# Kernel optimization log

Measured on AMD Instinct MI355X. Metric: run time of the kernel, lower is better.

Reference implementation:

```python
import jax, jax.numpy as jnp
import numpy as np

B, T, NF, C, H, TOPK = 4, 8, 8192, 384, 12, 32
D = C // H
SCALE = D ** -0.5  # qk_scale=None -> head_dim**-0.5


def setup_inputs() -> dict:
    key = jax.random.key(0)
    ks = jax.random.split(key, 4)
    x = jax.random.normal(ks[0], (B, T + NF, C), jnp.float32)
    qs_w = jax.random.normal(ks[1], (T, C, C), jnp.float32) * (C ** -0.5)
    kv_w = jax.random.normal(ks[2], (C, 2 * C), jnp.float32) * (C ** -0.5)
    experts_w = jax.random.normal(ks[3], (T, C, C), jnp.float32) * (C ** -0.5)
    return {"x": x, "qs_w": qs_w, "kv_w": kv_w, "experts_w": experts_w}


def reference(x, qs_w, kv_w, experts_w):
    # x: [B, T+NF, C]; first T tokens are task tokens, rest are feature tokens
    feature = x[:, T:, :]                                          # [B,NF,C]
    kv = (feature @ kv_w).reshape(B, NF, 2, H, D)                  # out dim splits [2,H,D]
    k = kv[:, :, 0].transpose(0, 2, 1, 3)                          # [B,H,NF,D]
    v = kv[:, :, 1].transpose(0, 2, 1, 3)                          # [B,H,NF,D]
    # per-task query linears (no bias), one task token each
    q = jnp.einsum('btc,tco->bto', x[:, :T, :], qs_w)              # [B,T,C]
    q = q.reshape(B, T, H, D).transpose(0, 2, 1, 3)                # [B,H,T,D]
    attn = jnp.einsum('bhtd,bhnd->bhtn', q, k) * SCALE             # [B,H,T,NF]
    vals, idx = jax.lax.top_k(attn, TOPK)                          # [B,H,T,K]
    w = jax.nn.softmax(vals, axis=-1)                              # softmax over top-k only
    # attn_token = (scatter(topk softmax) @ v) == weighted gather of v rows
    v_g = jnp.take_along_axis(v[:, :, None], idx[..., None], axis=3)   # [B,H,T,K,D]
    attn_token = jnp.einsum('bhtk,bhtkd->bhtd', w, v_g)
    attn_token = attn_token.transpose(0, 2, 1, 3).reshape(B, T, C)     # [B,T,C]
    # gather raw feature tokens at top-k indices, weight, scatter into padded zeros
    fm = feature.reshape(B, NF, H, D).transpose(0, 2, 1, 3)        # [B,H,NF,D]
    f_g = jnp.take_along_axis(fm[:, :, None], idx[..., None], axis=3) * w[..., None]  # [B,H,T,K,D]
    bi = jnp.arange(B)[:, None, None, None]
    hi = jnp.arange(H)[None, :, None, None]
    ti = jnp.arange(T)[None, None, :, None]
    # topk indices are unique per row -> set is well-defined
    feature_pad = jnp.zeros((B, H, T, NF, D), x.dtype).at[bi, hi, ti, idx].set(f_g)
    feature_pad = feature_pad.transpose(0, 2, 3, 1, 4).reshape(B, T, NF, C)  # [B,T,NF,C]
    # per-task expert linears; einsum with ones weight == sum over tasks
    feature_out = jnp.einsum('btnc,tco->bno', feature_pad, experts_w)  # [B,NF,C]
    token_out = jnp.einsum('btc,tco->bto', attn_token, experts_w)      # [B,T,C]
    return jnp.concatenate([token_out, feature_out], axis=1)          # [B,T+NF,C]
```

## Files before the change

### kernel.cpp

```cpp
#include <hip/hip_runtime.h>
#include <hip/hip_bf16.h>
#include <math.h>

#define B 4
#define T 8
#define NF 8192
#define C 384
#define H 12
#define TOPK 32
#define D 32
#define STOT (T + NF)
#define R (H * T)
#define KSEL 48
#define SCALE 0.17677669529663687f

typedef unsigned int uint;
typedef unsigned short ushort;
typedef short bf16x8 __attribute__((ext_vector_type(8)));
typedef float f32x4 __attribute__((ext_vector_type(4)));

__device__ __forceinline__ ushort bf16u(float a) {
  return __builtin_bit_cast(ushort, __float2bfloat16(a));
}

__device__ __forceinline__ ushort f32_key(float s) {
  uint kb = bf16u(s);
  kb ^= (kb & 0x8000u) ? 0xFFFFu : 0x8000u;
  return (ushort)kb;
}

__global__ __launch_bounds__(256) void ta_qproj_kernel(
    const float* __restrict__ x, const float* __restrict__ qs_w,
    float* __restrict__ q_part) {
  int t = blockIdx.x;
  int o0 = blockIdx.y * 64;
  int z = blockIdx.z;
  int tid = threadIdx.x;
  int o = tid & 63, ks = tid >> 6;
  __shared__ float xs[B][192];
  __shared__ float part[4][B][64];
  if (tid < 192) {
    int b = tid / 48, j4 = (tid % 48) * 4;
    *reinterpret_cast<float4*>(&xs[b][j4]) =
        *reinterpret_cast<const float4*>(x + ((size_t)b * STOT + t) * C + z * 192 + j4);
  }
  __syncthreads();
  float a0 = 0.f, a1 = 0.f, a2 = 0.f, a3 = 0.f;
  const float* w = qs_w + (size_t)t * C * C + (size_t)(z * 192 + ks * 48) * C + o0 + o;
#pragma unroll 8
  for (int c = 0; c < 48; ++c) {
    float wv = w[(size_t)c * C];
    int cj = ks * 48 + c;
    a0 += xs[0][cj] * wv;
    a1 += xs[1][cj] * wv;
    a2 += xs[2][cj] * wv;
    a3 += xs[3][cj] * wv;
  }
  part[ks][0][o] = a0; part[ks][1][o] = a1;
  part[ks][2][o] = a2; part[ks][3][o] = a3;
  __syncthreads();
  {
    int b = tid >> 6, oo = tid & 63;
    float s = part[0][b][oo] + part[1][b][oo] + part[2][b][oo] + part[3][b][oo];
    q_part[(((size_t)z * B + b) * T + t) * C + o0 + oo] = s;
  }
}

__global__ __launch_bounds__(384) void ta_fold_kernel(
    const float* __restrict__ q_part, const float* __restrict__ kv_w,
    float* __restrict__ qk_f32, ushort* __restrict__ qk_bf) {
  int b = blockIdx.x / H, h = blockIdx.x % H;
  int tid = threadIdx.x;
  __shared__ float kS[C][33];
  __shared__ float qh[T][D];
  if (tid < T * D) {
    int t = tid >> 5, d = tid & 31;
    qh[t][d] = q_part[((size_t)b * T + t) * C + h * D + d] +
               q_part[(((size_t)B + b) * T + t) * C + h * D + d];
  }
  for (int j = tid; j < C * 8; j += 384) {
    int c = j >> 3, d4 = (j & 7) * 4;
    float4 v = *reinterpret_cast<const float4*>(
        kv_w + (size_t)c * (2 * C) + h * D + d4);
    kS[c][d4 + 0] = v.x; kS[c][d4 + 1] = v.y;
    kS[c][d4 + 2] = v.z; kS[c][d4 + 3] = v.w;
  }
  __syncthreads();
  float acc[T] = {0.f, 0.f, 0.f, 0.f, 0.f, 0.f, 0.f, 0.f};
#pragma unroll
  for (int d = 0; d < D; ++d) {
    float kv = kS[tid][d];
#pragma unroll
    for (int t = 0; t < T; ++t) acc[t] += qh[t][d] * kv;
  }
#pragma unroll
  for (int t = 0; t < T; ++t) {
    size_t off = ((size_t)b * R + (size_t)h * T + t) * C + tid;
    float a = acc[t];
    qk_f32[off] = a;
    qk_bf[off] = bf16u(a);
  }
}

__global__ __launch_bounds__(256) void ta_scores_kernel(
    const float* __restrict__ x, const ushort* __restrict__ qk_bf,
    ushort* __restrict__ keys) {
  int b = blockIdx.y;
  int n0 = blockIdx.x * 64;
  int tid = threadIdx.x;
  int lane = tid & 63, w = tid >> 6;
  int row16 = lane & 15, kg = lane >> 4;
  __shared__ ushort fS[64][72];
  __shared__ ushort qS[96][72];
  f32x4 acc[6];
#pragma unroll
  for (int i = 0; i < 6; ++i) acc[i] = (f32x4){0.f, 0.f, 0.f, 0.f};

  const float* xb = x + ((size_t)b * STOT + T + n0) * C;
  const ushort* qb = qk_bf + (size_t)b * R * C;

  int frow = tid >> 2, fcg = (tid & 3) * 8;

#pragma unroll 1
  for (int c0 = 0; c0 < C; c0 += 32) {
    {
      const float* src = xb + (size_t)frow * C + c0 + fcg;
      float4 v0 = *reinterpret_cast<const float4*>(src);
      float4 v1 = *reinterpret_cast<const float4*>(src + 4);
      uint4 p;
      p.x = (uint)bf16u(v0.x) | ((uint)bf16u(v0.y) << 16);
      p.y = (uint)bf16u(v0.z) | ((uint)bf16u(v0.w) << 16);
      p.z = (uint)bf16u(v1.x) | ((uint)bf16u(v1.y) << 16);
      p.w = (uint)bf16u(v1.z) | ((uint)bf16u(v1.w) << 16);
      *reinterpret_cast<uint4*>(&fS[frow][fcg]) = p;
    }
#pragma unroll
    for (int s = 0; s < 2; ++s) {
      int u = tid + 256 * s;
      if (u < 384) {
        int row = u >> 2, cg = (u & 3) * 8;
        uint4 v = *reinterpret_cast<const uint4*>(qb + (size_t)row * C + c0 + cg);
        *reinterpret_cast<uint4*>(&qS[row][cg]) = v;
      }
    }
    __syncthreads();
    bf16x8 bfr = *reinterpret_cast<const bf16x8*>(&fS[w * 16 + row16][kg * 8]);
#pragma unroll
    for (int i = 0; i < 6; ++i) {
      bf16x8 afr = *reinterpret_cast<const bf16x8*>(&qS[i * 16 + row16][kg * 8]);
      acc[i] = __builtin_amdgcn_mfma_f32_16x16x32_bf16(afr, bfr, acc[i], 0, 0, 0);
    }
    __syncthreads();
  }
  int n = n0 + w * 16 + row16;
#pragma unroll
  for (int i = 0; i < 6; ++i) {
    int rbase = i * 16 + kg * 4;
#pragma unroll
    for (int reg = 0; reg < 4; ++reg) {
      keys[((size_t)b * R + rbase + reg) * NF + n] = f32_key(acc[i][reg] * SCALE);
    }
  }
}

__global__ __launch_bounds__(384) void ta_selres_kernel(
    const ushort* __restrict__ keys, const float* __restrict__ x,
    const float* __restrict__ qk_f32, float* __restrict__ w_buf,
    int* __restrict__ idx_buf, float4* __restrict__ out4) {
  int rr = blockIdx.x;
  int b = rr / R;
  int tid = threadIdx.x;
  int lane = tid & 63, wvi = tid >> 6;
  __shared__ __align__(16) ushort su[NF];
  __shared__ uint histW[6][256];
  __shared__ uint sh_prefix, sh_above, cgt, ceq;
  __shared__ int gt_list[KSEL];
  __shared__ int eq_list[128];
  __shared__ int il[KSEL];
  __shared__ float sv[KSEL];
  __shared__ int rkS[KSEL];
  __shared__ float qS[C];
  __shared__ float smax, esum;

  {
    const uint4* src = reinterpret_cast<const uint4*>(keys + (size_t)rr * NF);
    uint4* dst = reinterpret_cast<uint4*>(su);
    for (int j = tid; j < NF / 8; j += 384) dst[j] = src[j];
  }
  {
    float4 z = {0.f, 0.f, 0.f, 0.f};
    float4* dst = out4 + (size_t)rr * (B * STOT * C / 4 / (B * R));
    for (int j = tid; j < B * STOT * C / 4 / (B * R); j += 384) dst[j] = z;
  }
  qS[tid] = qk_f32[(size_t)rr * C + tid];
  for (int i = tid; i < 6 * 256; i += 384) (&histW[0][0])[i] = 0;
  if (tid == 0) { cgt = 0; ceq = 0; }
  __syncthreads();

  for (int i = tid; i < NF; i += 384) atomicAdd(&histW[wvi][su[i] >> 8], 1u);
  __syncthreads();
  if (tid < 64) {
    uint h0 = 0, h1 = 0, h2 = 0, h3 = 0;
#pragma unroll
    for (int wq = 0; wq < 6; ++wq) {
      h0 += histW[wq][4 * lane + 0];
      h1 += histW[wq][4 * lane + 1];
      h2 += histW[wq][4 * lane + 2];
      h3 += histW[wq][4 * lane + 3];
    }
    uint lsum = h0 + h1 + h2 + h3;
    uint suf = lsum;
#pragma unroll
    for (int off = 1; off < 64; off <<= 1) {
      uint o = __shfl_down(suf, off);
      if (lane + off < 64) suf += o;
    }
    uint gn3 = suf - lsum;
    uint ge3 = gn3 + h3;
    uint ge2 = ge3 + h2;
    uint ge1 = ge2 + h1;
    uint ge0 = ge1 + h0;
    const uint need = KSEL;
    if (ge0 >= need && ge1 < need) { sh_prefix = 4 * lane + 0; sh_above = ge1; }
    if (ge1 >= need && ge2 < need) { sh_prefix = 4 * lane + 1; sh_above = ge2; }
    if (ge2 >= need && ge3 < need) { sh_prefix = 4 * lane + 2; sh_above = ge3; }
    if (ge3 >= need && gn3 < need) { sh_prefix = 4 * lane + 3; sh_above = gn3; }
  }
  __syncthreads();
  uint pref1 = sh_prefix, ab1 = sh_above;
  for (int i = tid; i < 6 * 256; i += 384) (&histW[0][0])[i] = 0;
  __syncthreads();
  for (int i = tid; i < NF; i += 384) {
    uint u = su[i];
    if ((u >> 8) == pref1) atomicAdd(&histW[wvi][u & 255], 1u);
  }
  __syncthreads();
  if (tid < 64) {
    uint h0 = 0, h1 = 0, h2 = 0, h3 = 0;
#pragma unroll
    for (int wq = 0; wq < 6; ++wq) {
      h0 += histW[wq][4 * lane + 0];
      h1 += histW[wq][4 * lane + 1];
      h2 += histW[wq][4 * lane + 2];
      h3 += histW[wq][4 * lane + 3];
    }
    uint lsum = h0 + h1 + h2 + h3;
    uint suf = lsum;
#pragma unroll
    for (int off = 1; off < 64; off <<= 1) {
      uint o = __shfl_down(suf, off);
      if (lane + off < 64) suf += o;
    }
    uint gn3 = suf - lsum;
    uint ge3 = gn3 + h3;
    uint ge2 = ge3 + h2;
    uint ge1 = ge2 + h1;
    uint ge0 = ge1 + h0;
    const uint need = (uint)KSEL - ab1;
    if (ge0 >= need && ge1 < need) { sh_prefix = (pref1 << 8) | (4 * lane + 0); sh_above = ab1 + ge1; }
    if (ge1 >= need && ge2 < need) { sh_prefix = (pref1 << 8) | (4 * lane + 1); sh_above = ab1 + ge2; }
    if (ge2 >= need && ge3 < need) { sh_prefix = (pref1 << 8) | (4 * lane + 2); sh_above = ab1 + ge3; }
    if (ge3 >= need && gn3 < need) { sh_prefix = (pref1 << 8) | (4 * lane + 3); sh_above = ab1 + gn3; }
  }
  __syncthreads();
  uint piv = sh_prefix, ab = sh_above;
  for (int i = tid; i < NF; i += 384) {
    uint u = su[i];
    if (u > piv) {
      uint s = atomicAdd(&cgt, 1u);
      gt_list[s] = i;
    } else if (u == piv) {
      uint s = atomicAdd(&ceq, 1u);
      if (s < 128) eq_list[s] = i;
    }
  }
  __syncthreads();
  if (tid < (int)ab) il[tid] = gt_list[tid];
  {
    uint ne = ceq < 128u ? ceq : 128u;
    if (tid < (int)ne) {
      int my = eq_list[tid];
      int r2 = 0;
      for (uint e = 0; e < ne; ++e) r2 += (eq_list[e] < my);
      if (r2 < (int)((uint)KSEL - ab)) il[ab + r2] = my;
    }
  }
  __syncthreads();

  int k = tid >> 3, j = tid & 7;
  const float* fp = x + ((size_t)b * STOT + T + il[k]) * C + j;
  float s = 0.f;
#pragma unroll 8
  for (int m = 0; m < 48; ++m) s += fp[m * 8] * qS[j + m * 8];
  s += __shfl_down(s, 4);
  s += __shfl_down(s, 2);
  s += __shfl_down(s, 1);
  if (j == 0) sv[k] = s * SCALE;
  __syncthreads();
  if (tid < KSEL) {
    float mys = sv[tid];
    int myn = il[tid];
    int r = 0;
#pragma unroll
    for (int e = 0; e < KSEL; ++e) {
      float se = sv[e];
      r += (se > mys) || (se == mys && il[e] < myn);
    }
    rkS[tid] = r;
    if (r == 0) smax = mys;
  }
  __syncthreads();
  float e = 0.f;
  if (tid < KSEL && rkS[tid] < TOPK) e = expf(sv[tid] - smax);
  if (tid < 64) {
    float t2 = e;
#pragma unroll
    for (int off = 32; off; off >>= 1) t2 += __shfl_down(t2, off);
    if (tid == 0) esum = t2;
  }
  __syncthreads();
  if (tid < KSEL && rkS[tid] < TOPK) {
    w_buf[(size_t)rr * TOPK + rkS[tid]] = e / esum;
    idx_buf[(size_t)rr * TOPK + rkS[tid]] = il[tid];
  }
}

__global__ __launch_bounds__(256) void ta_gvscatter_kernel(
    const float* __restrict__ x, const float* __restrict__ kv_w,
    const float* __restrict__ ew, const float* __restrict__ w_buf,
    const int* __restrict__ idx_buf, float* __restrict__ out) {
  int br = blockIdx.x;
  int t = br % T, h = (br / T) % H, b = br / R;
  int tid = threadIdx.x;
  int k = tid >> 3, dg = tid & 7;
  __shared__ float Fc[TOPK][100];
  __shared__ float Vc[96][36];
  __shared__ float vS[TOPK][36];
  __shared__ float gS[TOPK][36];
  __shared__ __align__(16) float attS[D];
  __shared__ float wl[TOPK];
  __shared__ int il[TOPK];

  if (tid < TOPK) {
    wl[tid] = w_buf[(size_t)br * TOPK + tid];
    il[tid] = idx_buf[(size_t)br * TOPK + tid];
  }
  __syncthreads();
  float4 acc = {0.f, 0.f, 0.f, 0.f};
  int hc = (h * D) / 96;
#pragma unroll 1
  for (int ch = 0; ch < 4; ++ch) {
    int c0 = ch * 96;
    if (ch) __syncthreads();
#pragma unroll
    for (int s = 0; s < 3; ++s) {
      int u = tid + 256 * s;
      int kr = u / 24, c4 = (u % 24) * 4;
      *reinterpret_cast<float4*>(&Fc[kr][c4]) =
          *reinterpret_cast<const float4*>(
              x + ((size_t)b * STOT + T + il[kr]) * C + c0 + c4);
    }
#pragma unroll
    for (int s = 0; s < 3; ++s) {
      int u = tid + 256 * s;
      int cr = u >> 3, d4 = (u & 7) * 4;
      *reinterpret_cast<float4*>(&Vc[cr][d4]) =
          *reinterpret_cast<const float4*>(
              kv_w + (size_t)(c0 + cr) * (2 * C) + C + h * D + d4);
    }
    __syncthreads();
    if (ch == hc) {
      int off = h * D - c0;
      float4 f = *reinterpret_cast<const float4*>(&Fc[k][off + 4 * dg]);
      float wk = wl[k];
      float4 g = {wk * f.x, wk * f.y, wk * f.z, wk * f.w};
      *reinterpret_cast<float4*>(&gS[k][4 * dg]) = g;
    }
#pragma unroll 4
    for (int c = 0; c < 96; c += 4) {
      float4 f4 = *reinterpret_cast<const float4*>(&Fc[k][c]);
      float4 v0 = *reinterpret_cast<const float4*>(&Vc[c + 0][4 * dg]);
      float4 v1 = *reinterpret_cast<const float4*>(&Vc[c + 1][4 * dg]);
      float4 v2 = *reinterpret_cast<const float4*>(&Vc[c + 2][4 * dg]);
      float4 v3 = *reinterpret_cast<const float4*>(&Vc[c + 3][4 * dg]);
      acc.x += f4.x * v0.x + f4.y * v1.x + f4.z * v2.x + f4.w * v3.x;
      acc.y += f4.x * v0.y + f4.y * v1.y + f4.z * v2.y + f4.w * v3.y;
      acc.z += f4.x * v0.z + f4.y * v1.z + f4.z * v2.z + f4.w * v3.z;
      acc.w += f4.x * v0.w + f4.y * v1.w + f4.z * v2.w + f4.w * v3.w;
    }
  }
  *reinterpret_cast<float4*>(&vS[k][4 * dg]) = acc;
  __syncthreads();
  if (tid < D) {
    float a = 0.f;
#pragma unroll
    for (int kk = 0; kk < TOPK; ++kk) a += wl[kk] * vS[kk][tid];
    attS[tid] = a;
  }
  __syncthreads();

  float ewc0[D], ewc1[D];
  const float* ewt = ew + (size_t)t * C * C + (size_t)h * D * C;
#pragma unroll
  for (int dd = 0; dd < D; ++dd) {
    ewc0[dd] = ewt[(size_t)dd * C + tid];
    ewc1[dd] = (tid < 128) ? ewt[(size_t)dd * C + tid + 256] : 0.f;
  }
  size_t obase = (size_t)b * STOT * C;
#pragma unroll 1
  for (int kk = 0; kk < TOPK; ++kk) {
    float y0 = 0.f, y1 = 0.f;
#pragma unroll
    for (int d4 = 0; d4 < D; d4 += 4) {
      float4 g4 = *reinterpret_cast<const float4*>(&gS[kk][d4]);
      y0 += g4.x * ewc0[d4] + g4.y * ewc0[d4 + 1] +
            g4.z * ewc0[d4 + 2] + g4.w * ewc0[d4 + 3];
      y1 += g4.x * ewc1[d4] + g4.y * ewc1[d4 + 1] +
            g4.z * ewc1[d4 + 2] + g4.w * ewc1[d4 + 3];
    }
    size_t row = obase + (size_t)(T + il[kk]) * C;
    atomicAdd(&out[row + tid], y0);
    if (tid < 128) atomicAdd(&out[row + tid + 256], y1);
  }
  {
    float y0 = 0.f, y1 = 0.f;
#pragma unroll
    for (int d4 = 0; d4 < D; d4 += 4) {
      float4 a4 = *reinterpret_cast<const float4*>(attS + d4);
      y0 += a4.x * ewc0[d4] + a4.y * ewc0[d4 + 1] +
            a4.z * ewc0[d4 + 2] + a4.w * ewc0[d4 + 3];
      y1 += a4.x * ewc1[d4] + a4.y * ewc1[d4 + 1] +
            a4.z * ewc1[d4 + 2] + a4.w * ewc1[d4 + 3];
    }
    size_t row = obase + (size_t)t * C;
    atomicAdd(&out[row + tid], y0);
    if (tid < 128) atomicAdd(&out[row + tid + 256], y1);
  }
}

extern "C" void kernel_launch(void* const* d_in, const int* in_sizes, int n_in,
                              void* d_out, int out_size, void* d_ws, size_t ws_size,
                              hipStream_t stream) {
  const float* x = (const float*)d_in[0];
  const float* qs_w = (const float*)d_in[1];
  const float* kv_w = (const float*)d_in[2];
  const float* ew = (const float*)d_in[3];
  float* out = (float*)d_out;

  char* p = (char*)d_ws;
  float* qk_f32 = (float*)p;  p += (size_t)B * R * C * 4;
  ushort* qk_bf = (ushort*)p; p += (size_t)B * R * C * 2;
  ushort* keys = (ushort*)p;  p += (size_t)B * R * NF * 2;
  float* w_buf = (float*)p;   p += (size_t)B * R * TOPK * 4;
  int* idx_buf = (int*)p;     p += (size_t)B * R * TOPK * 4;
  float* q_part = (float*)p;

  dim3 gq(T, C / 64, 2);
  ta_qproj_kernel<<<gq, 256, 0, stream>>>(x, qs_w, q_part);
  ta_fold_kernel<<<B * H, 384, 0, stream>>>(q_part, kv_w, qk_f32, qk_bf);
  dim3 g2(NF / 64, B);
  ta_scores_kernel<<<g2, 256, 0, stream>>>(x, qk_bf, keys);
  ta_selres_kernel<<<B * R, 384, 0, stream>>>(keys, x, qk_f32, w_buf, idx_buf,
                                              (float4*)out);
  ta_gvscatter_kernel<<<B * R, 256, 0, stream>>>(x, kv_w, ew, w_buf, idx_buf, out);
}
```

Before: 88.77 us.

## Fuse top-k selection with gather/scatter kernel and move output zeroing into scores

Merges the selection/softmax kernel and the gather-V/expert-scatter kernel into one 256-thread kernel, with a shared-memory union so the selection buffers and the gather tiles reuse the same LDS. Weights and indices stay in shared memory instead of going through global w_buf/idx_buf, which removes one launch and a round trip through memory. The zeroing of the output moves into the scores kernel's 512 blocks, spreading it across more blocks. In exchange the selection phase runs with fewer threads per block (256 instead of 384), and the fused block's larger LDS use may lower occupancy.

```diff
diff --git a/kernel.cpp b/kernel.cpp
--- a/kernel.cpp
+++ b/kernel.cpp
@@ -104,7 +104,7 @@
 
 __global__ __launch_bounds__(256) void ta_scores_kernel(
     const float* __restrict__ x, const ushort* __restrict__ qk_bf,
-    ushort* __restrict__ keys) {
+    ushort* __restrict__ keys, float4* __restrict__ out4) {
   int b = blockIdx.y;
   int n0 = blockIdx.x * 64;
   int tid = threadIdx.x;
@@ -115,6 +115,14 @@
   f32x4 acc[6];
 #pragma unroll
   for (int i = 0; i < 6; ++i) acc[i] = (f32x4){0.f, 0.f, 0.f, 0.f};
+
+  {
+    const int SL = (B * STOT * C / 4) / 512;
+    int zbid = blockIdx.y * gridDim.x + blockIdx.x;
+    float4 z = {0.f, 0.f, 0.f, 0.f};
+    float4* dst = out4 + (size_t)zbid * SL;
+    for (int j = tid; j < SL; j += 256) dst[j] = z;
+  }
 
   const float* xb = x + ((size_t)b * STOT + T + n0) * C;
   const ushort* qb = qk_bf + (size_t)b * R * C;
@@ -163,50 +171,60 @@
   }
 }
 
-__global__ __launch_bounds__(384) void ta_selres_kernel(
+__global__ __launch_bounds__(256) void ta_selgv_kernel(
     const ushort* __restrict__ keys, const float* __restrict__ x,
-    const float* __restrict__ qk_f32, float* __restrict__ w_buf,
-    int* __restrict__ idx_buf, float4* __restrict__ out4) {
-  int rr = blockIdx.x;
-  int b = rr / R;
+    const float* __restrict__ qk_f32, const float* __restrict__ kv_w,
+    const float* __restrict__ ew, float* __restrict__ out) {
+  int br = blockIdx.x;
+  int t = br % T, h = (br / T) % H, b = br / R;
   int tid = threadIdx.x;
   int lane = tid & 63, wvi = tid >> 6;
-  __shared__ __align__(16) ushort su[NF];
-  __shared__ uint histW[6][256];
+
+  union SM {
+    struct {
+      ushort su[NF];
+      uint histW[4][256];
+      float qS[C];
+      int gt_list[KSEL];
+      int eq_list[128];
+      int il[KSEL];
+      float sv[KSEL];
+      int rkS[KSEL];
+    } a;
+    struct {
+      float Fc[TOPK][100];
+      float Vc[96][36];
+    } g;
+  };
+  __shared__ SM sm;
+  __shared__ float vS[TOPK][36];
+  __shared__ float gS[TOPK][36];
+  __shared__ __align__(16) float attS[D];
+  __shared__ float wl[TOPK];
+  __shared__ int top_il[TOPK];
   __shared__ uint sh_prefix, sh_above, cgt, ceq;
-  __shared__ int gt_list[KSEL];
-  __shared__ int eq_list[128];
-  __shared__ int il[KSEL];
-  __shared__ float sv[KSEL];
-  __shared__ int rkS[KSEL];
-  __shared__ float qS[C];
   __shared__ float smax, esum;
 
   {
-    const uint4* src = reinterpret_cast<const uint4*>(keys + (size_t)rr * NF);
-    uint4* dst = reinterpret_cast<uint4*>(su);
-    for (int j = tid; j < NF / 8; j += 384) dst[j] = src[j];
-  }
-  {
-    float4 z = {0.f, 0.f, 0.f, 0.f};
-    float4* dst = out4 + (size_t)rr * (B * STOT * C / 4 / (B * R));
-    for (int j = tid; j < B * STOT * C / 4 / (B * R); j += 384) dst[j] = z;
-  }
-  qS[tid] = qk_f32[(size_t)rr * C + tid];
-  for (int i = tid; i < 6 * 256; i += 384) (&histW[0][0])[i] = 0;
+    const uint4* src = reinterpret_cast<const uint4*>(keys + (size_t)br * NF);
+    uint4* dst = reinterpret_cast<uint4*>(sm.a.su);
+    for (int j = tid; j < NF / 8; j += 256) dst[j] = src[j];
+  }
+  for (int j = tid; j < C; j += 256) sm.a.qS[j] = qk_f32[(size_t)br * C + j];
+  for (int i = tid; i < 4 * 256; i += 256) (&sm.a.histW[0][0])[i] = 0;
   if (tid == 0) { cgt = 0; ceq = 0; }
   __syncthreads();
 
-  for (int i = tid; i < NF; i += 384) atomicAdd(&histW[wvi][su[i] >> 8], 1u);
+  for (int i = tid; i < NF; i += 256) atomicAdd(&sm.a.histW[wvi][sm.a.su[i] >> 8], 1u);
   __syncthreads();
   if (tid < 64) {
     uint h0 = 0, h1 = 0, h2 = 0, h3 = 0;
 #pragma unroll
-    for (int wq = 0; wq < 6; ++wq) {
-      h0 += histW[wq][4 * lane + 0];
-      h1 += histW[wq][4 * lane + 1];
-      h2 += histW[wq][4 * lane + 2];
-      h3 += histW[wq][4 * lane + 3];
+    for (int wq = 0; wq < 4; ++wq) {
+      h0 += sm.a.histW[wq][4 * lane + 0];
+      h1 += sm.a.histW[wq][4 * lane + 1];
+      h2 += sm.a.histW[wq][4 * lane + 2];
+      h3 += sm.a.histW[wq][4 * lane + 3];
     }
     uint lsum = h0 + h1 + h2 + h3;
     uint suf = lsum;
@@ -228,21 +246,21 @@
   }
   __syncthreads();
   uint pref1 = sh_prefix, ab1 = sh_above;
-  for (int i = tid; i < 6 * 256; i += 384) (&histW[0][0])[i] = 0;
-  __syncthreads();
-  for (int i = tid; i < NF; i += 384) {
-    uint u = su[i];
-    if ((u >> 8) == pref1) atomicAdd(&histW[wvi][u & 255], 1u);
+  for (int i = tid; i < 4 * 256; i += 256) (&sm.a.histW[0][0])[i] = 0;
+  __syncthreads();
+  for (int i = tid; i < NF; i += 256) {
+    uint u = sm.a.su[i];
+    if ((u >> 8) == pref1) atomicAdd(&sm.a.histW[wvi][u & 255], 1u);
   }
   __syncthreads();
   if (tid < 64) {
     uint h0 = 0, h1 = 0, h2 = 0, h3 = 0;
 #pragma unroll
-    for (int wq = 0; wq < 6; ++wq) {
-      h0 += histW[wq][4 * lane + 0];
-      h1 += histW[wq][4 * lane + 1];
-      h2 += histW[wq][4 * lane + 2];
-      h3 += histW[wq][4 * lane + 3];
+    for (int wq = 0; wq < 4; ++wq) {
+      h0 += sm.a.histW[wq][4 * lane + 0];
+      h1 += sm.a.histW[wq][4 * lane + 1];
+      h2 += sm.a.histW[wq][4 * lane + 2];
+      h3 += sm.a.histW[wq][4 * lane + 3];
     }
     uint lsum = h0 + h1 + h2 + h3;
     uint suf = lsum;
@@ -264,88 +282,83 @@
   }
   __syncthreads();
   uint piv = sh_prefix, ab = sh_above;
-  for (int i = tid; i < NF; i += 384) {
-    uint u = su[i];
+  for (int i = tid; i < NF; i += 256) {
+    uint u = sm.a.su[i];
     if (u > piv) {
       uint s = atomicAdd(&cgt, 1u);
-      gt_list[s] = i;
+      sm.a.gt_list[s] = i;
     } else if (u == piv) {
       uint s = atomicAdd(&ceq, 1u);
-      if (s < 128) eq_list[s] = i;
-    }
-  }
-  __syncthreads();
-  if (tid < (int)ab) il[tid] = gt_list[tid];
+      if (s < 128) sm.a.eq_list[s] = i;
+    }
+  }
+  __syncthreads();
+  if (tid < (int)ab) sm.a.il[tid] = sm.a.gt_list[tid];
   {
     uint ne = ceq < 128u ? ceq : 128u;
     if (tid < (int)ne) {
-      int my = eq_list[tid];
+      int my = sm.a.eq_list[tid];
       int r2 = 0;
-      for (uint e = 0; e < ne; ++e) r2 += (eq_list[e] < my);
-      if (r2 < (int)((uint)KSEL - ab)) il[ab + r2] = my;
-    }
-  }
-  __syncthreads();
-
-  int k = tid >> 3, j = tid & 7;
-  const float* fp = x + ((size_t)b * STOT + T + il[k]) * C + j;
-  float s = 0.f;
+      for (uint e = 0; e < ne; ++e) r2 += (sm.a.eq_list[e] < my);
+      if (r2 < (int)((uint)KSEL - ab)) sm.a.il[ab + r2] = my;
+    }
+  }
+  __syncthreads();
+
+  {
+    int k = tid >> 3, j = tid & 7;
+    const float* fp = x + ((size_t)b * STOT + T + sm.a.il[k]) * C + j;
+    float s = 0.f;
 #pragma unroll 8
-  for (int m = 0; m < 48; ++m) s += fp[m * 8] * qS[j + m * 8];
-  s += __shfl_down(s, 4);
-  s += __shfl_down(s, 2);
-  s += __shfl_down(s, 1);
-  if (j == 0) sv[k] = s * SCALE;
+    for (int m = 0; m < 48; ++m) s += fp[m * 8] * sm.a.qS[j + m * 8];
+    s += __shfl_down(s, 4);
+    s += __shfl_down(s, 2);
+    s += __shfl_down(s, 1);
+    if (j == 0) sm.a.sv[k] = s * SCALE;
+  }
+  if (tid < 128) {
+    int k = 32 + (tid >> 3), j = tid & 7;
+    const float* fp = x + ((size_t)b * STOT + T + sm.a.il[k]) * C + j;
+    float s = 0.f;
+#pragma unroll 8
+    for (int m = 0; m < 48; ++m) s += fp[m * 8] * sm.a.qS[j + m * 8];
+    s += __shfl_down(s, 4);
+    s += __shfl_down(s, 2);
+    s += __shfl_down(s, 1);
+    if (j == 0) sm.a.sv[k] = s * SCALE;
+  }
   __syncthreads();
   if (tid < KSEL) {
-    float mys = sv[tid];
-    int myn = il[tid];
+    float mys = sm.a.sv[tid];
+    int myn = sm.a.il[tid];
     int r = 0;
 #pragma unroll
     for (int e = 0; e < KSEL; ++e) {
-      float se = sv[e];
-      r += (se > mys) || (se == mys && il[e] < myn);
-    }
-    rkS[tid] = r;
+      float se = sm.a.sv[e];
+      r += (se > mys) || (se == mys && sm.a.il[e] < myn);
+    }
+    sm.a.rkS[tid] = r;
     if (r == 0) smax = mys;
   }
   __syncthreads();
-  float e = 0.f;
-  if (tid < KSEL && rkS[tid] < TOPK) e = expf(sv[tid] - smax);
-  if (tid < 64) {
-    float t2 = e;
-#pragma unroll
-    for (int off = 32; off; off >>= 1) t2 += __shfl_down(t2, off);
-    if (tid == 0) esum = t2;
-  }
-  __syncthreads();
-  if (tid < KSEL && rkS[tid] < TOPK) {
-    w_buf[(size_t)rr * TOPK + rkS[tid]] = e / esum;
-    idx_buf[(size_t)rr * TOPK + rkS[tid]] = il[tid];
-  }
-}
-
-__global__ __launch_bounds__(256) void ta_gvscatter_kernel(
-    const float* __restrict__ x, const float* __restrict__ kv_w,
-    const float* __restrict__ ew, const float* __restrict__ w_buf,
-    const int* __restrict__ idx_buf, float* __restrict__ out) {
-  int br = blockIdx.x;
-  int t = br % T, h = (br / T) % H, b = br / R;
-  int tid = threadIdx.x;
+  {
+    float e = 0.f;
+    if (tid < KSEL && sm.a.rkS[tid] < TOPK) e = expf(sm.a.sv[tid] - smax);
+    if (tid < 64) {
+      float t2 = e;
+#pragma unroll
+      for (int off = 32; off; off >>= 1) t2 += __shfl_down(t2, off);
+      if (tid == 0) esum = t2;
+    }
+    __syncthreads();
+    if (tid < KSEL && sm.a.rkS[tid] < TOPK) {
+      wl[sm.a.rkS[tid]] = e / esum;
+      top_il[sm.a.rkS[tid]] = sm.a.il[tid];
+    }
+  }
+  __syncthreads();
+
   int k = tid >> 3, dg = tid & 7;
-  __shared__ float Fc[TOPK][100];
-  __shared__ float Vc[96][36];
-  __shared__ float vS[TOPK][36];
-  __shared__ float gS[TOPK][36];
-  __shared__ __align__(16) float attS[D];
-  __shared__ float wl[TOPK];
-  __shared__ int il[TOPK];
-
-  if (tid < TOPK) {
-    wl[tid] = w_buf[(size_t)br * TOPK + tid];
-    il[tid] = idx_buf[(size_t)br * TOPK + tid];
-  }
-  __syncthreads();
   float4 acc = {0.f, 0.f, 0.f, 0.f};
   int hc = (h * D) / 96;
 #pragma unroll 1
@@ -356,33 +369,33 @@
     for (int s = 0; s < 3; ++s) {
       int u = tid + 256 * s;
       int kr = u / 24, c4 = (u % 24) * 4;
-      *reinterpret_cast<float4*>(&Fc[kr][c4]) =
+      *reinterpret_cast<float4*>(&sm.g.Fc[kr][c4]) =
           *reinterpret_cast<const float4*>(
-              x + ((size_t)b * STOT + T + il[kr]) * C + c0 + c4);
+              x + ((size_t)b * STOT + T + top_il[kr]) * C + c0 + c4);
     }
 #pragma unroll
     for (int s = 0; s < 3; ++s) {
       int u = tid + 256 * s;
       int cr = u >> 3, d4 = (u & 7) * 4;
-      *reinterpret_cast<float4*>(&Vc[cr][d4]) =
+      *reinterpret_cast<float4*>(&sm.g.Vc[cr][d4]) =
           *reinterpret_cast<const float4*>(
               kv_w + (size_t)(c0 + cr) * (2 * C) + C + h * D + d4);
     }
     __syncthreads();
     if (ch == hc) {
       int off = h * D - c0;
-      float4 f = *reinterpret_cast<const float4*>(&Fc[k][off + 4 * dg]);
+      float4 f = *reinterpret_cast<const float4*>(&sm.g.Fc[k][off + 4 * dg]);
       float wk = wl[k];
       float4 g = {wk * f.x, wk * f.y, wk * f.z, wk * f.w};
       *reinterpret_cast<float4*>(&gS[k][4 * dg]) = g;
     }
 #pragma unroll 4
     for (int c = 0; c < 96; c += 4) {
-      float4 f4 = *reinterpret_cast<const float4*>(&Fc[k][c]);
-      float4 v0 = *reinterpret_cast<const float4*>(&Vc[c + 0][4 * dg]);
-      float4 v1 = *reinterpret_cast<const float4*>(&Vc[c + 1][4 * dg]);
-      float4 v2 = *reinterpret_cast<const float4*>(&Vc[c + 2][4 * dg]);
-      float4 v3 = *reinterpret_cast<const float4*>(&Vc[c + 3][4 * dg]);
+      float4 f4 = *reinterpret_cast<const float4*>(&sm.g.Fc[k][c]);
+      float4 v0 = *reinterpret_cast<const float4*>(&sm.g.Vc[c + 0][4 * dg]);
+      float4 v1 = *reinterpret_cast<const float4*>(&sm.g.Vc[c + 1][4 * dg]);
+      float4 v2 = *reinterpret_cast<const float4*>(&sm.g.Vc[c + 2][4 * dg]);
+      float4 v3 = *reinterpret_cast<const float4*>(&sm.g.Vc[c + 3][4 * dg]);
       acc.x += f4.x * v0.x + f4.y * v1.x + f4.z * v2.x + f4.w * v3.x;
       acc.y += f4.x * v0.y + f4.y * v1.y + f4.z * v2.y + f4.w * v3.y;
       acc.z += f4.x * v0.z + f4.y * v1.z + f4.z * v2.z + f4.w * v3.z;
@@ -418,7 +431,7 @@
       y1 += g4.x * ewc1[d4] + g4.y * ewc1[d4 + 1] +
             g4.z * ewc1[d4 + 2] + g4.w * ewc1[d4 + 3];
     }
-    size_t row = obase + (size_t)(T + il[kk]) * C;
+    size_t row = obase + (size_t)(T + top_il[kk]) * C;
     atomicAdd(&out[row + tid], y0);
     if (tid < 128) atomicAdd(&out[row + tid + 256], y1);
   }
@@ -451,16 +464,12 @@
   float* qk_f32 = (float*)p;  p += (size_t)B * R * C * 4;
   ushort* qk_bf = (ushort*)p; p += (size_t)B * R * C * 2;
   ushort* keys = (ushort*)p;  p += (size_t)B * R * NF * 2;
-  float* w_buf = (float*)p;   p += (size_t)B * R * TOPK * 4;
-  int* idx_buf = (int*)p;     p += (size_t)B * R * TOPK * 4;
   float* q_part = (float*)p;
 
   dim3 gq(T, C / 64, 2);
   ta_qproj_kernel<<<gq, 256, 0, stream>>>(x, qs_w, q_part);
   ta_fold_kernel<<<B * H, 384, 0, stream>>>(q_part, kv_w, qk_f32, qk_bf);
   dim3 g2(NF / 64, B);
-  ta_scores_kernel<<<g2, 256, 0, stream>>>(x, qk_bf, keys);
-  ta_selres_kernel<<<B * R, 384, 0, stream>>>(keys, x, qk_f32, w_buf, idx_buf,
-                                              (float4*)out);
-  ta_gvscatter_kernel<<<B * R, 256, 0, stream>>>(x, kv_w, ew, w_buf, idx_buf, out);
-}
+  ta_scores_kernel<<<g2, 256, 0, stream>>>(x, qk_bf, keys, (float4*)out);
+  ta_selgv_kernel<<<B * R, 256, 0, stream>>>(keys, x, qk_f32, kv_w, ew, out);
+}
```

New measurement: 93.21 us. +5.0%, slower.

## Single-pass 12-bit top-k select, move output zeroing, split gather-scatter across halves

Applied to the files above, without the earlier changes.

The two-pass 8-bit radix selection in the selection kernel becomes a single 4096-bin histogram pass. Every element in or above the pivot bucket is packed as a (key, index) candidate and ranked by pairwise comparison, which drops one histogram pass and several barriers. Zeroing of the output buffer moves from the 384-block selection kernel into the 512-block scores kernel, taking bulk stores off the selection kernel's critical path. The gather/scatter kernel is split so each row's top-k set is handled by two blocks of 16 items, doubling grid parallelism at the cost of reloading the Vc tiles twice and adding more atomic traffic.

```diff
diff --git a/kernel.cpp b/kernel.cpp
--- a/kernel.cpp
+++ b/kernel.cpp
@@ -18,6 +18,7 @@
 typedef unsigned short ushort;
 typedef short bf16x8 __attribute__((ext_vector_type(8)));
 typedef float f32x4 __attribute__((ext_vector_type(4)));
+typedef float f32x2 __attribute__((ext_vector_type(2)));
 
 __device__ __forceinline__ ushort bf16u(float a) {
   return __builtin_bit_cast(ushort, __float2bfloat16(a));
@@ -104,7 +105,7 @@
 
 __global__ __launch_bounds__(256) void ta_scores_kernel(
     const float* __restrict__ x, const ushort* __restrict__ qk_bf,
-    ushort* __restrict__ keys) {
+    ushort* __restrict__ keys, float4* __restrict__ out4) {
   int b = blockIdx.y;
   int n0 = blockIdx.x * 64;
   int tid = threadIdx.x;
@@ -115,6 +116,14 @@
   f32x4 acc[6];
 #pragma unroll
   for (int i = 0; i < 6; ++i) acc[i] = (f32x4){0.f, 0.f, 0.f, 0.f};
+
+  {
+    const int SL = (B * STOT * C / 4) / 512;
+    int zbid = blockIdx.y * gridDim.x + blockIdx.x;
+    float4 z = {0.f, 0.f, 0.f, 0.f};
+    float4* dst = out4 + (size_t)zbid * SL;
+    for (int j = tid; j < SL; j += 256) dst[j] = z;
+  }
 
   const float* xb = x + ((size_t)b * STOT + T + n0) * C;
   const ushort* qb = qk_bf + (size_t)b * R * C;
@@ -166,16 +175,16 @@
 __global__ __launch_bounds__(384) void ta_selres_kernel(
     const ushort* __restrict__ keys, const float* __restrict__ x,
     const float* __restrict__ qk_f32, float* __restrict__ w_buf,
-    int* __restrict__ idx_buf, float4* __restrict__ out4) {
+    int* __restrict__ idx_buf) {
   int rr = blockIdx.x;
   int b = rr / R;
   int tid = threadIdx.x;
   int lane = tid & 63, wvi = tid >> 6;
   __shared__ __align__(16) ushort su[NF];
-  __shared__ uint histW[6][256];
-  __shared__ uint sh_prefix, sh_above, cgt, ceq;
-  __shared__ int gt_list[KSEL];
-  __shared__ int eq_list[128];
+  __shared__ uint hist[4096];
+  __shared__ uint cand[1024];
+  __shared__ uint wtot[4];
+  __shared__ uint sh_piv, sh_above, cnt;
   __shared__ int il[KSEL];
   __shared__ float sv[KSEL];
   __shared__ int rkS[KSEL];
@@ -187,102 +196,61 @@
     uint4* dst = reinterpret_cast<uint4*>(su);
     for (int j = tid; j < NF / 8; j += 384) dst[j] = src[j];
   }
-  {
-    float4 z = {0.f, 0.f, 0.f, 0.f};
-    float4* dst = out4 + (size_t)rr * (B * STOT * C / 4 / (B * R));
-    for (int j = tid; j < B * STOT * C / 4 / (B * R); j += 384) dst[j] = z;
-  }
   qS[tid] = qk_f32[(size_t)rr * C + tid];
-  for (int i = tid; i < 6 * 256; i += 384) (&histW[0][0])[i] = 0;
-  if (tid == 0) { cgt = 0; ceq = 0; }
-  __syncthreads();
-
-  for (int i = tid; i < NF; i += 384) atomicAdd(&histW[wvi][su[i] >> 8], 1u);
-  __syncthreads();
-  if (tid < 64) {
-    uint h0 = 0, h1 = 0, h2 = 0, h3 = 0;
-#pragma unroll
-    for (int wq = 0; wq < 6; ++wq) {
-      h0 += histW[wq][4 * lane + 0];
-      h1 += histW[wq][4 * lane + 1];
-      h2 += histW[wq][4 * lane + 2];
-      h3 += histW[wq][4 * lane + 3];
-    }
-    uint lsum = h0 + h1 + h2 + h3;
-    uint suf = lsum;
+  for (int i = tid; i < 4096; i += 384) hist[i] = 0;
+  if (tid == 0) cnt = 0;
+  __syncthreads();
+
+  for (int i = tid; i < NF; i += 384) atomicAdd(&hist[su[i] >> 4], 1u);
+  __syncthreads();
+
+  uint pp = 0, suf = 0;
+  if (tid < 256) {
+#pragma unroll
+    for (int j = 0; j < 16; ++j) pp += hist[tid * 16 + j];
+    suf = pp;
 #pragma unroll
     for (int off = 1; off < 64; off <<= 1) {
       uint o = __shfl_down(suf, off);
       if (lane + off < 64) suf += o;
     }
-    uint gn3 = suf - lsum;
-    uint ge3 = gn3 + h3;
-    uint ge2 = ge3 + h2;
-    uint ge1 = ge2 + h1;
-    uint ge0 = ge1 + h0;
-    const uint need = KSEL;
-    if (ge0 >= need && ge1 < need) { sh_prefix = 4 * lane + 0; sh_above = ge1; }
-    if (ge1 >= need && ge2 < need) { sh_prefix = 4 * lane + 1; sh_above = ge2; }
-    if (ge2 >= need && ge3 < need) { sh_prefix = 4 * lane + 2; sh_above = ge3; }
-    if (ge3 >= need && gn3 < need) { sh_prefix = 4 * lane + 3; sh_above = gn3; }
-  }
-  __syncthreads();
-  uint pref1 = sh_prefix, ab1 = sh_above;
-  for (int i = tid; i < 6 * 256; i += 384) (&histW[0][0])[i] = 0;
-  __syncthreads();
+    if (lane == 0) wtot[wvi] = suf;
+  }
+  __syncthreads();
+  if (tid < 256) {
+    uint later = 0;
+    for (int wq = wvi + 1; wq < 4; ++wq) later += wtot[wq];
+    uint geg = later + suf;
+    uint gng = geg - pp;
+    if (geg >= (uint)KSEL && gng < (uint)KSEL) {
+      uint run = gng;
+      int pv = 0; uint ab = 0;
+      for (int j = 15; j >= 0; --j) {
+        uint c = hist[tid * 16 + j];
+        uint nrun = run + c;
+        if (nrun >= (uint)KSEL && run < (uint)KSEL) { pv = tid * 16 + j; ab = run; }
+        run = nrun;
+      }
+      sh_piv = (uint)pv; sh_above = ab;
+    }
+  }
+  __syncthreads();
+  uint piv = sh_piv;
   for (int i = tid; i < NF; i += 384) {
     uint u = su[i];
-    if ((u >> 8) == pref1) atomicAdd(&histW[wvi][u & 255], 1u);
-  }
-  __syncthreads();
-  if (tid < 64) {
-    uint h0 = 0, h1 = 0, h2 = 0, h3 = 0;
-#pragma unroll
-    for (int wq = 0; wq < 6; ++wq) {
-      h0 += histW[wq][4 * lane + 0];
-      h1 += histW[wq][4 * lane + 1];
-      h2 += histW[wq][4 * lane + 2];
-      h3 += histW[wq][4 * lane + 3];
-    }
-    uint lsum = h0 + h1 + h2 + h3;
-    uint suf = lsum;
-#pragma unroll
-    for (int off = 1; off < 64; off <<= 1) {
-      uint o = __shfl_down(suf, off);
-      if (lane + off < 64) suf += o;
-    }
-    uint gn3 = suf - lsum;
-    uint ge3 = gn3 + h3;
-    uint ge2 = ge3 + h2;
-    uint ge1 = ge2 + h1;
-    uint ge0 = ge1 + h0;
-    const uint need = (uint)KSEL - ab1;
-    if (ge0 >= need && ge1 < need) { sh_prefix = (pref1 << 8) | (4 * lane + 0); sh_above = ab1 + ge1; }
-    if (ge1 >= need && ge2 < need) { sh_prefix = (pref1 << 8) | (4 * lane + 1); sh_above = ab1 + ge2; }
-    if (ge2 >= need && ge3 < need) { sh_prefix = (pref1 << 8) | (4 * lane + 2); sh_above = ab1 + ge3; }
-    if (ge3 >= need && gn3 < need) { sh_prefix = (pref1 << 8) | (4 * lane + 3); sh_above = ab1 + gn3; }
-  }
-  __syncthreads();
-  uint piv = sh_prefix, ab = sh_above;
-  for (int i = tid; i < NF; i += 384) {
-    uint u = su[i];
-    if (u > piv) {
-      uint s = atomicAdd(&cgt, 1u);
-      gt_list[s] = i;
-    } else if (u == piv) {
-      uint s = atomicAdd(&ceq, 1u);
-      if (s < 128) eq_list[s] = i;
-    }
-  }
-  __syncthreads();
-  if (tid < (int)ab) il[tid] = gt_list[tid];
+    if ((u >> 4) >= piv) {
+      uint s = atomicAdd(&cnt, 1u);
+      if (s < 1024) cand[s] = (u << 13) | (8191u - (uint)i);
+    }
+  }
+  __syncthreads();
   {
-    uint ne = ceq < 128u ? ceq : 128u;
-    if (tid < (int)ne) {
-      int my = eq_list[tid];
-      int r2 = 0;
-      for (uint e = 0; e < ne; ++e) r2 += (eq_list[e] < my);
-      if (r2 < (int)((uint)KSEL - ab)) il[ab + r2] = my;
+    uint m = cnt < 1024u ? cnt : 1024u;
+    if (tid < (int)m) {
+      uint me = cand[tid];
+      int r = 0;
+      for (uint e = 0; e < m; ++e) r += (cand[e] > me);
+      if (r < KSEL) il[r] = 8191 - (int)(me & 8191u);
     }
   }
   __syncthreads();
@@ -291,7 +259,7 @@
   const float* fp = x + ((size_t)b * STOT + T + il[k]) * C + j;
   float s = 0.f;
 #pragma unroll 8
-  for (int m = 0; m < 48; ++m) s += fp[m * 8] * qS[j + m * 8];
+  for (int m2 = 0; m2 < 48; ++m2) s += fp[m2 * 8] * qS[j + m2 * 8];
   s += __shfl_down(s, 4);
   s += __shfl_down(s, 2);
   s += __shfl_down(s, 1);
@@ -329,36 +297,39 @@
     const float* __restrict__ x, const float* __restrict__ kv_w,
     const float* __restrict__ ew, const float* __restrict__ w_buf,
     const int* __restrict__ idx_buf, float* __restrict__ out) {
-  int br = blockIdx.x;
+  constexpr int KH = TOPK / 2;
+  int br = blockIdx.x >> 1, half = blockIdx.x & 1;
   int t = br % T, h = (br / T) % H, b = br / R;
   int tid = threadIdx.x;
-  int k = tid >> 3, dg = tid & 7;
-  __shared__ float Fc[TOPK][100];
+  int k16 = tid >> 4, lane16 = tid & 15, d0 = 2 * lane16;
+  __shared__ float Fc[KH][100];
   __shared__ float Vc[96][36];
-  __shared__ float vS[TOPK][36];
-  __shared__ float gS[TOPK][36];
+  __shared__ float vS[KH][36];
+  __shared__ float gS[KH][36];
   __shared__ __align__(16) float attS[D];
-  __shared__ float wl[TOPK];
-  __shared__ int il[TOPK];
-
-  if (tid < TOPK) {
-    wl[tid] = w_buf[(size_t)br * TOPK + tid];
-    il[tid] = idx_buf[(size_t)br * TOPK + tid];
-  }
-  __syncthreads();
-  float4 acc = {0.f, 0.f, 0.f, 0.f};
+  __shared__ float wl[KH];
+  __shared__ int il[KH];
+
+  if (tid < KH) {
+    wl[tid] = w_buf[(size_t)br * TOPK + half * KH + tid];
+    il[tid] = idx_buf[(size_t)br * TOPK + half * KH + tid];
+  }
+  __syncthreads();
+  f32x2 acc = {0.f, 0.f};
   int hc = (h * D) / 96;
 #pragma unroll 1
   for (int ch = 0; ch < 4; ++ch) {
     int c0 = ch * 96;
     if (ch) __syncthreads();
 #pragma unroll
-    for (int s = 0; s < 3; ++s) {
+    for (int s = 0; s < 2; ++s) {
       int u = tid + 256 * s;
-      int kr = u / 24, c4 = (u % 24) * 4;
-      *reinterpret_cast<float4*>(&Fc[kr][c4]) =
-          *reinterpret_cast<const float4*>(
-              x + ((size_t)b * STOT + T + il[kr]) * C + c0 + c4);
+      if (u < 384) {
+        int kr = u / 24, c4 = (u % 24) * 4;
+        *reinterpret_cast<float4*>(&Fc[kr][c4]) =
+            *reinterpret_cast<const float4*>(
+                x + ((size_t)b * STOT + T + il[kr]) * C + c0 + c4);
+      }
     }
 #pragma unroll
     for (int s = 0; s < 3; ++s) {
@@ -371,30 +342,29 @@
     __syncthreads();
     if (ch == hc) {
       int off = h * D - c0;
-      float4 f = *reinterpret_cast<const float4*>(&Fc[k][off + 4 * dg]);
-      float wk = wl[k];
-      float4 g = {wk * f.x, wk * f.y, wk * f.z, wk * f.w};
-      *reinterpret_cast<float4*>(&gS[k][4 * dg]) = g;
+      f32x2 f = *reinterpret_cast<const f32x2*>(&Fc[k16][off + d0]);
+      float wk = wl[k16];
+      gS[k16][d0] = wk * f.x;
+      gS[k16][d0 + 1] = wk * f.y;
     }
 #pragma unroll 4
     for (int c = 0; c < 96; c += 4) {
-      float4 f4 = *reinterpret_cast<const float4*>(&Fc[k][c]);
-      float4 v0 = *reinterpret_cast<const float4*>(&Vc[c + 0][4 * dg]);
-      float4 v1 = *reinterpret_cast<const float4*>(&Vc[c + 1][4 * dg]);
-      float4 v2 = *reinterpret_cast<const float4*>(&Vc[c + 2][4 * dg]);
-      float4 v3 = *reinterpret_cast<const float4*>(&Vc[c + 3][4 * dg]);
+      float4 f4 = *reinterpret_cast<const float4*>(&Fc[k16][c]);
+      f32x2 v0 = *reinterpret_cast<const f32x2*>(&Vc[c + 0][d0]);
+      f32x2 v1 = *reinterpret_cast<const f32x2*>(&Vc[c + 1][d0]);
+      f32x2 v2 = *reinterpret_cast<const f32x2*>(&Vc[c + 2][d0]);
+      f32x2 v3 = *reinterpret_cast<const f32x2*>(&Vc[c + 3][d0]);
       acc.x += f4.x * v0.x + f4.y * v1.x + f4.z * v2.x + f4.w * v3.x;
       acc.y += f4.x * v0.y + f4.y * v1.y + f4.z * v2.y + f4.w * v3.y;
-      acc.z += f4.x * v0.z + f4.y * v1.z + f4.z * v2.z + f4.w * v3.z;
-      acc.w += f4.x * v0.w + f4.y * v1.w + f4.z * v2.w + f4.w * v3.w;
-    }
-  }
-  *reinterpret_cast<float4*>(&vS[k][4 * dg]) = acc;
+    }
+  }
+  vS[k16][d0] = acc.x;
+  vS[k16][d0 + 1] = acc.y;
   __syncthreads();
   if (tid < D) {
     float a = 0.f;
 #pragma unroll
-    for (int kk = 0; kk < TOPK; ++kk) a += wl[kk] * vS[kk][tid];
+    for (int kk = 0; kk < KH; ++kk) a += wl[kk] * vS[kk][tid];
     attS[tid] = a;
   }
   __syncthreads();
@@ -408,7 +378,7 @@
   }
   size_t obase = (size_t)b * STOT * C;
 #pragma unroll 1
-  for (int kk = 0; kk < TOPK; ++kk) {
+  for (int kk = 0; kk < KH; ++kk) {
     float y0 = 0.f, y1 = 0.f;
 #pragma unroll
     for (int d4 = 0; d4 < D; d4 += 4) {
@@ -459,8 +429,7 @@
   ta_qproj_kernel<<<gq, 256, 0, stream>>>(x, qs_w, q_part);
   ta_fold_kernel<<<B * H, 384, 0, stream>>>(q_part, kv_w, qk_f32, qk_bf);
   dim3 g2(NF / 64, B);
-  ta_scores_kernel<<<g2, 256, 0, stream>>>(x, qk_bf, keys);
-  ta_selres_kernel<<<B * R, 384, 0, stream>>>(keys, x, qk_f32, w_buf, idx_buf,
-                                              (float4*)out);
-  ta_gvscatter_kernel<<<B * R, 256, 0, stream>>>(x, kv_w, ew, w_buf, idx_buf, out);
-}
+  ta_scores_kernel<<<g2, 256, 0, stream>>>(x, qk_bf, keys, (float4*)out);
+  ta_selres_kernel<<<B * R, 384, 0, stream>>>(keys, x, qk_f32, w_buf, idx_buf);
+  ta_gvscatter_kernel<<<B * R * 2, 256, 0, stream>>>(x, kv_w, ew, w_buf, idx_buf, out);
+}
```

Result: no change. 87.64 us (-1.3%).
